# Kernel optimization log

Measured on AMD Instinct MI355X. Metric: run time of the kernel, lower is better.

## Reference

```python
import jax, jax.numpy as jnp
import numpy as np

B, T, DIM, FF, E, TOPK = 2, 2048, 1024, 4096, 8, 2


def setup_inputs() -> dict:
    key = jax.random.key(0)
    k0, k1, k2, k3 = jax.random.split(key, 4)
    x = jax.random.normal(k0, (B, T, DIM), jnp.float32)
    # router weight [E, D] (nn.Linear(dim, num_experts, bias=False))
    Wr = jax.random.normal(k1, (E, DIM), jnp.float32) * (DIM ** -0.5)
    # per-expert FFN weights, stacked: W1 [E, D, FF], W2 [E, FF, D]
    W1 = jax.random.normal(k2, (E, DIM, FF), jnp.float32) * (DIM ** -0.5)
    W2 = jax.random.normal(k3, (E, FF, DIM), jnp.float32) * (FF ** -0.5)
    return {"x": x, "Wr": Wr, "W1": W1, "W2": W2}


def reference(x, Wr, W1, W2):
    """MoEFeedForward.forward, world_size=1, STANDARD implementation.

    Math: per token, top_k experts by router logits, softmax over the top_k
    logits (fp32), y = sum_k w_k * FFN_{e_k}(x). The torch code realizes this
    via sort/permute + per-expert variable-size GEMM + weighted index_add;
    the scatter-add result is identical to the dense masked form below,
    which is the jit-friendly (static-shape) expression.
    """
    Bn, Tn, D = x.shape
    num_experts = Wr.shape[0]
    xf = x.reshape(-1, D)                      # [N, D], N = B*T
    N = xf.shape[0]

    logits = xf @ Wr.T                         # [N, E]
    topw, topi = jax.lax.top_k(logits, TOPK)   # [N, K]
    topw = jax.nn.softmax(topw.astype(jnp.float32), axis=-1).astype(x.dtype)

    # combine weight for each (token, expert): [N, E] (0 if not routed)
    combine = jnp.zeros((N, num_experts), x.dtype)
    combine = combine.at[jnp.arange(N)[:, None], topi].add(topw)

    out = jnp.zeros_like(xf)
    for e in range(num_experts):               # fixed small loop over experts
        h = jax.nn.gelu(xf @ W1[e], approximate=False)  # exact GELU (nn.GELU)
        out = out + combine[:, e:e + 1] * (h @ W2[e])
    return out.reshape(Bn, Tn, D)
```

## Files before the change

kernel.cpp:

```cpp
#include <hip/hip_runtime.h>
#include <hip/hip_bf16.h>
#include <hip/hip_fp16.h>

#define NTOK 4096
#define DIM 1024
#define FF 4096
#define NE 8
#define NSLOT 8192

typedef _Float16 half8 __attribute__((ext_vector_type(8)));
typedef _Float16 half4 __attribute__((ext_vector_type(4)));
typedef float floatx4 __attribute__((ext_vector_type(4)));

__device__ __forceinline__ float gelu_exact(float x) {
    return 0.5f * x * (1.0f + erff(x * 0.70710678118654752f));
}

__device__ __forceinline__ void gl_lds16(const void* g, void* l) {
    __builtin_amdgcn_global_load_lds(
        (const __attribute__((address_space(1))) void*)g,
        (__attribute__((address_space(3))) void*)l, 16, 0, 0);
}

__device__ __forceinline__ void transpose_tile128(const float* __restrict__ s,
                                                  _Float16* __restrict__ d,
                                                  int R, int C, int r0, int c0,
                                                  char* smem) {
    float* t = (float*)smem;
    int tid = threadIdx.x;
    int rr = tid >> 4, cc = (tid & 15) * 4;
#pragma unroll
    for (int i = 0; i < 8; ++i) {
        int r = rr + i * 16;
        float4 v = *(const float4*)(s + (size_t)(r0 + r) * C + c0 + cc);
        *(float4*)(t + r * 64 + (cc ^ (((r >> 3) & 15) << 2))) = v;
    }
    __syncthreads();
#pragma unroll
    for (int j = 0; j < 4; ++j) {
        int chunk = j * 256 + tid;
        int fr = chunk >> 4, ch = chunk & 15;
        half8 v;
#pragma unroll
        for (int u = 0; u < 8; ++u)
            v[u] = (_Float16)t[(ch * 8 + u) * 64 + (fr ^ (ch << 2))];
        *(half8*)(d + (size_t)(c0 + fr) * R + r0 + ch * 8) = v;
    }
}

__global__ __launch_bounds__(256) void k_prep(
    const float* __restrict__ x,
    const float* __restrict__ Wr,
    const float* __restrict__ W1,
    _Float16* __restrict__ w1t,
    _Float16* __restrict__ xh,
    int* __restrict__ counts,
    int* __restrict__ tok_e,
    float* __restrict__ tok_w,
    int* __restrict__ tok_pos) {
    __shared__ char smem[32768];
    int bid = blockIdx.x;
    int tid = threadIdx.x;
    int q = bid / 7, r = bid % 7;
    if (r < 4) {
        int t = q * 4 + r;
        int e = t >> 9, rem = t & 511;
        int r0 = (rem >> 6) << 7, c0 = (rem & 63) << 6;
        transpose_tile128(W1 + (size_t)e * DIM * FF, w1t + (size_t)e * FF * DIM,
                          DIM, FF, r0, c0, smem);
    } else if (r < 6) {
        int i = (q * 2 + (r - 4)) * 2048 + tid * 8;
        float4 a = *(const float4*)(x + i);
        float4 b = *(const float4*)(x + i + 4);
        half8 h;
        h[0] = (_Float16)a.x; h[1] = (_Float16)a.y; h[2] = (_Float16)a.z; h[3] = (_Float16)a.w;
        h[4] = (_Float16)b.x; h[5] = (_Float16)b.y; h[6] = (_Float16)b.z; h[7] = (_Float16)b.w;
        *(half8*)(xh + i) = h;
    } else {
        float* wr = (float*)smem;
        for (int i = tid; i < NE * DIM / 4; i += 256)
            ((float4*)wr)[i] = ((const float4*)Wr)[i];
        __syncthreads();
        int w = tid >> 6, lane = tid & 63;
        int t = q * 4 + w;
        float acc[NE] = {};
        for (int j = 0; j < DIM / 64; ++j) {
            float xv = x[t * DIM + j * 64 + lane];
#pragma unroll
            for (int e = 0; e < NE; ++e)
                acc[e] += xv * wr[e * DIM + j * 64 + lane];
        }
#pragma unroll
        for (int e = 0; e < NE; ++e) {
#pragma unroll
            for (int s = 32; s; s >>= 1) acc[e] += __shfl_xor(acc[e], s, 64);
        }
        if (lane == 0) {
            int b0 = 0; float m0 = acc[0];
#pragma unroll
            for (int e = 1; e < NE; ++e) { if (acc[e] > m0) { m0 = acc[e]; b0 = e; } }
            int b1 = -1; float m1 = -1e30f;
#pragma unroll
            for (int e = 0; e < NE; ++e) { if (e != b0 && acc[e] > m1) { m1 = acc[e]; b1 = e; } }
            float z = __expf(m1 - m0);
            float zz = 1.0f / (1.0f + z);
            int p0 = atomicAdd(&counts[b0], 1);
            int p1 = atomicAdd(&counts[b1], 1);
            tok_e[2 * t] = b0;  tok_e[2 * t + 1] = b1;
            tok_w[2 * t] = zz;  tok_w[2 * t + 1] = z * zz;
            tok_pos[2 * t] = p0; tok_pos[2 * t + 1] = p1;
        }
    }
}

__global__ __launch_bounds__(256) void k_transpose(const float* __restrict__ src,
                                                   _Float16* __restrict__ dst,
                                                   int R, int C) {
    __shared__ float t[64][65];
    int e = blockIdx.z;
    const float* s = src + (size_t)e * R * C;
    _Float16* d = dst + (size_t)e * C * R;
    int r0 = blockIdx.y * 64, c0 = blockIdx.x * 64;
    int tid = threadIdx.x;
    int rr = tid >> 4, cc = (tid & 15) * 4;
#pragma unroll
    for (int i = 0; i < 4; ++i) {
        float4 v = *(const float4*)(s + (size_t)(r0 + rr + i * 16) * C + c0 + cc);
        t[rr + i * 16][cc] = v.x; t[rr + i * 16][cc + 1] = v.y;
        t[rr + i * 16][cc + 2] = v.z; t[rr + i * 16][cc + 3] = v.w;
    }
    __syncthreads();
    int f = tid >> 3, ch = tid & 7;
#pragma unroll
    for (int j = 0; j < 2; ++j) {
        int fr = f + j * 32;
        half8 v;
#pragma unroll
        for (int u = 0; u < 8; ++u) v[u] = (_Float16)t[ch * 8 + u][fr];
        *(half8*)(d + (size_t)(c0 + fr) * R + r0 + ch * 8) = v;
    }
}

__global__ __launch_bounds__(256) void k_prefix_slots(
    const int* __restrict__ counts, int* __restrict__ offs,
    int* __restrict__ tmap256, int* __restrict__ tmap128,
    const int* __restrict__ tok_e, const int* __restrict__ tok_pos,
    int* __restrict__ tok_slot, int* __restrict__ list_tok) {
    __shared__ int soffs[NE];
    if (threadIdx.x == 0) {
        int s = 0, n2 = 0, n1 = 0;
        for (int e = 0; e < NE; ++e) {
            offs[e] = s; soffs[e] = s;
            int c = counts[e];
            for (int mt = 0; mt * 256 < c; ++mt) tmap256[1 + n2++] = (e << 16) | mt;
            for (int mt = 0; mt * 128 < c; ++mt) tmap128[1 + n1++] = (e << 16) | mt;
            s += c;
        }
        offs[NE] = s;
        tmap256[0] = n2;
        tmap128[0] = n1;
    }
    __syncthreads();
    for (int idx = threadIdx.x; idx < NSLOT; idx += 256) {
        int e = tok_e[idx];
        int slot = soffs[e] + tok_pos[idx];
        tok_slot[idx] = slot;
        list_tok[slot] = idx >> 1;
    }
}

template<int K, int NOUT, bool GATHER, bool GELU>
__device__ __forceinline__ void ffn128_body(
    const _Float16* __restrict__ Abase,
    const _Float16* __restrict__ Wbase,
    const int* __restrict__ counts,
    const int* __restrict__ offs,
    const int* __restrict__ list_tok,
    _Float16* __restrict__ Out,
    int e, int mt, int f0, _Float16* lds) {

    int base = offs[e] + mt * 128;
    int valid = counts[e] - mt * 128;

    int tid = threadIdx.x;
    int wid = tid >> 6, lane = tid & 63;

    const char* AB = (const char*)Abase;
    const char* WB = (const char*)(Wbase + (size_t)e * NOUT * K);

    size_t aoff[4]; unsigned boff[4];
#pragma unroll
    for (int i = 0; i < 4; ++i) {
        int g = wid * 256 + i * 64 + lane;
        int r = g >> 3;
        int c = (g & 7) ^ (r & 7);
        int rr = (r < valid) ? r : (valid - 1);
        unsigned arow = GATHER ? (unsigned)list_tok[base + rr] : (unsigned)(base + rr);
        aoff[i] = (size_t)arow * (K * 2) + c * 16;
        boff[i] = (unsigned)(f0 + r) * (unsigned)(K * 2) + c * 16;
    }

    floatx4 acc[4][4];
#pragma unroll
    for (int m = 0; m < 4; ++m)
#pragma unroll
        for (int n = 0; n < 4; ++n) acc[m][n] = (floatx4){0.f, 0.f, 0.f, 0.f};

    int la = lane & 15, lb = lane >> 4;
    int wm = (wid >> 1) * 64, wn = (wid & 1) * 64;

#pragma unroll
    for (int i = 0; i < 4; ++i)
        gl_lds16(AB + aoff[i], lds + wid * 2048 + i * 512);
#pragma unroll
    for (int i = 0; i < 4; ++i)
        gl_lds16(WB + boff[i], lds + 16384 + wid * 2048 + i * 512);
    asm volatile("s_waitcnt vmcnt(0)" ::: "memory");
    __builtin_amdgcn_s_barrier();
    __builtin_amdgcn_sched_barrier(0);

    constexpr int NT = K / 64;
#pragma unroll 2
    for (int t = 0; t < NT; ++t) {
        int cur = t & 1;
        if (t + 1 < NT) {
            size_t kadv = (size_t)(t + 1) * 128;
            _Float16* Ad = lds + (cur ^ 1) * 8192;
            _Float16* Bd = lds + 16384 + (cur ^ 1) * 8192;
#pragma unroll
            for (int i = 0; i < 4; ++i)
                gl_lds16(AB + aoff[i] + kadv, Ad + wid * 2048 + i * 512);
#pragma unroll
            for (int i = 0; i < 4; ++i)
                gl_lds16(WB + boff[i] + kadv, Bd + wid * 2048 + i * 512);
        }
        const _Float16* Ac = lds + cur * 8192;
        const _Float16* Bc = lds + 16384 + cur * 8192;
#pragma unroll
        for (int kk = 0; kk < 2; ++kk) {
            half8 af[4], bf[4];
#pragma unroll
            for (int m = 0; m < 4; ++m) {
                int row = wm + m * 16 + la;
                int c = kk * 4 + lb;
                af[m] = *(const half8*)(Ac + row * 64 + ((c ^ (row & 7)) * 8));
            }
#pragma unroll
            for (int n = 0; n < 4; ++n) {
                int row = wn + n * 16 + la;
                int c = kk * 4 + lb;
                bf[n] = *(const half8*)(Bc + row * 64 + ((c ^ (row & 7)) * 8));
            }
#pragma unroll
            for (int m = 0; m < 4; ++m)
#pragma unroll
                for (int n = 0; n < 4; ++n)
                    acc[m][n] = __builtin_amdgcn_mfma_f32_16x16x32_f16(af[m], bf[n], acc[m][n], 0, 0, 0);
        }
        __builtin_amdgcn_sched_barrier(0);
        asm volatile("s_waitcnt vmcnt(0)" ::: "memory");
        __builtin_amdgcn_s_barrier();
        __builtin_amdgcn_sched_barrier(0);
    }

    _Float16* tw = lds + wid * 4096;
#pragma unroll
    for (int m = 0; m < 4; ++m)
#pragma unroll
        for (int n = 0; n < 4; ++n) {
            floatx4 v = acc[m][n];
#pragma unroll
            for (int i = 0; i < 4; ++i) {
                float fv = v[i];
                if (GELU) fv = gelu_exact(fv);
                tw[(m * 16 + lb * 4 + i) * 64 + n * 16 + la] = (_Float16)fv;
            }
        }
    asm volatile("s_waitcnt lgkmcnt(0)" ::: "memory");
    __builtin_amdgcn_sched_barrier(0);
#pragma unroll
    for (int i = 0; i < 8; ++i) {
        int gi = i * 64 + lane;
        int row = gi >> 3, c8 = gi & 7;
        half8 v = *(const half8*)(tw + gi * 8);
        int trow = wm + row;
        if (trow < valid)
            *(half8*)(Out + (size_t)(base + trow) * NOUT + f0 + wn + c8 * 8) = v;
    }
}

template<int K, int NOUT, bool GATHER, bool GELU>
__global__ __launch_bounds__(256) void k_ffn(
    const _Float16* __restrict__ Abase,
    const _Float16* __restrict__ Wbase,
    const int* __restrict__ tmap,
    const int* __restrict__ counts,
    const int* __restrict__ offs,
    const int* __restrict__ list_tok,
    _Float16* __restrict__ Out) {
    __shared__ _Float16 lds[32768];
    int nt_m = tmap[0];
    if ((int)blockIdx.x >= nt_m) return;
    int ent = tmap[1 + blockIdx.x];
    ffn128_body<K, NOUT, GATHER, GELU>(Abase, Wbase, counts, offs, list_tok, Out,
                                       ent >> 16, ent & 0xffff, blockIdx.y * 128, lds);
}

__global__ __launch_bounds__(256) void k_ffn1_fused(
    const _Float16* __restrict__ xh,
    const _Float16* __restrict__ w1t,
    const int* __restrict__ tmap,
    const int* __restrict__ counts,
    const int* __restrict__ offs,
    const int* __restrict__ list_tok,
    _Float16* __restrict__ hbuf,
    const float* __restrict__ W2,
    _Float16* __restrict__ w2t) {
    __shared__ _Float16 lds[32768];
    int bid = blockIdx.x;
    int q = bid / 10, r = bid % 10;
    if (r < 2) {
        int f = q * 2 + r;
        int nt_m = tmap[0];
        int tile = f >> 5;
        if (tile >= nt_m) return;
        int ent = tmap[1 + tile];
        ffn128_body<DIM, FF, true, true>(xh, w1t, counts, offs, list_tok, hbuf,
                                         ent >> 16, ent & 0xffff, (f & 31) * 128, lds);
    } else {
        int t = q * 8 + (r - 2);
        if (t >= 8 * 32 * 16) return;
        int e = t >> 9, rem = t & 511;
        int r0 = (rem >> 4) << 7, c0 = (rem & 15) << 6;
        transpose_tile128(W2 + (size_t)e * FF * DIM, w2t + (size_t)e * DIM * FF,
                          FF, DIM, r0, c0, (char*)lds);
    }
}

template<int K, int NOUT, int KSPAN, bool GATHER, bool GELU>
__global__ __launch_bounds__(512, 2) void k_ffn256(
    const _Float16* __restrict__ Abase,
    const _Float16* __restrict__ Wbase,
    const int* __restrict__ tmap,
    const int* __restrict__ counts,
    const int* __restrict__ offs,
    const int* __restrict__ list_tok,
    _Float16* __restrict__ Out) {

    int nt_m = tmap[0];
    if ((int)blockIdx.x >= nt_m) return;
    int ent = tmap[1 + blockIdx.x];
    int e = ent >> 16, mt = ent & 0xffff;
    int base = offs[e] + mt * 256;
    int valid = counts[e] - mt * 256;
    int f0 = blockIdx.y * 256;
    int kbase = blockIdx.z * KSPAN;
    Out += (size_t)blockIdx.z * ((size_t)NSLOT * NOUT);

    __shared__ _Float16 lds[65536];

    int tid = threadIdx.x;
    int wid = tid >> 6, lane = tid & 63;

    const char* AB = (const char*)Abase;
    const char* WB = (const char*)(Wbase + (size_t)e * NOUT * K);

    size_t aoff[4]; unsigned boff[4];
#pragma unroll
    for (int i = 0; i < 4; ++i) {
        int g = i * 512 + tid;
        int r = g >> 3;
        int c = (g & 7) ^ (r & 7);
        int rr = (r < valid) ? r : (valid - 1);
        unsigned arow = GATHER ? (unsigned)list_tok[base + rr] : (unsigned)(base + rr);
        aoff[i] = (size_t)arow * (K * 2) + c * 16 + (size_t)kbase * 2;
        boff[i] = (unsigned)(f0 + r) * (unsigned)(K * 2) + c * 16 + (unsigned)kbase * 2;
    }

    floatx4 acc[8][4];
#pragma unroll
    for (int m = 0; m < 8; ++m)
#pragma unroll
        for (int n = 0; n < 4; ++n) acc[m][n] = (floatx4){0.f, 0.f, 0.f, 0.f};

    int la = lane & 15, lb = lane >> 4;
    int wmb = (wid >> 2) * 128, wnb = (wid & 3) * 64;

#pragma unroll
    for (int i = 0; i < 4; ++i)
        gl_lds16(AB + aoff[i], lds + i * 4096 + wid * 512);
#pragma unroll
    for (int i = 0; i < 4; ++i)
        gl_lds16(WB + boff[i], lds + 32768 + i * 4096 + wid * 512);
    asm volatile("s_waitcnt vmcnt(0)" ::: "memory");
    __builtin_amdgcn_s_barrier();
    __builtin_amdgcn_sched_barrier(0);

    constexpr int NT = KSPAN / 64;
#pragma unroll 2
    for (int t = 0; t < NT; ++t) {
        int cur = t & 1;
        if (t + 1 < NT) {
            size_t adv = (size_t)(t + 1) * 128;
            _Float16* Ad = lds + (cur ^ 1) * 16384;
            _Float16* Bd = lds + 32768 + (cur ^ 1) * 16384;
#pragma unroll
            for (int i = 0; i < 4; ++i)
                gl_lds16(AB + aoff[i] + adv, Ad + i * 4096 + wid * 512);
#pragma unroll
            for (int i = 0; i < 4; ++i)
                gl_lds16(WB + boff[i] + adv, Bd + i * 4096 + wid * 512);
        }
        const _Float16* Ac = lds + cur * 16384;
        const _Float16* Bc = lds + 32768 + cur * 16384;
#pragma unroll
        for (int kk = 0; kk < 2; ++kk) {
            half8 af[8], bf[4];
#pragma unroll
            for (int n = 0; n < 4; ++n) {
                int row = wnb + n * 16 + la;
                int c = kk * 4 + lb;
                bf[n] = *(const half8*)(Bc + row * 64 + ((c ^ (row & 7)) * 8));
            }
#pragma unroll
            for (int m = 0; m < 8; ++m) {
                int row = wmb + m * 16 + la;
                int c = kk * 4 + lb;
                af[m] = *(const half8*)(Ac + row * 64 + ((c ^ (row & 7)) * 8));
            }
#pragma unroll
            for (int m = 0; m < 8; ++m)
#pragma unroll
                for (int n = 0; n < 4; ++n)
                    acc[m][n] = __builtin_amdgcn_mfma_f32_16x16x32_f16(af[m], bf[n], acc[m][n], 0, 0, 0);
        }
        __builtin_amdgcn_sched_barrier(0);
        asm volatile("s_waitcnt vmcnt(0)" ::: "memory");
        __builtin_amdgcn_s_barrier();
        __builtin_amdgcn_sched_barrier(0);
    }

    _Float16* tw = lds + wid * 4096;
#pragma unroll
    for (int ps = 0; ps < 2; ++ps) {
#pragma unroll
        for (int fi = 0; fi < 4; ++fi)
#pragma unroll
            for (int nf = 0; nf < 4; ++nf) {
                floatx4 v = acc[ps * 4 + fi][nf];
#pragma unroll
                for (int i2 = 0; i2 < 4; ++i2) {
                    float fv = v[i2];
                    if (GELU) fv = gelu_exact(fv);
                    tw[(fi * 16 + lb * 4 + i2) * 64 + nf * 16 + la] = (_Float16)fv;
                }
            }
        asm volatile("s_waitcnt lgkmcnt(0)" ::: "memory");
        __builtin_amdgcn_sched_barrier(0);
#pragma unroll
        for (int i2 = 0; i2 < 8; ++i2) {
            int gi = i2 * 64 + lane;
            int row = gi >> 3, c8 = gi & 7;
            half8 v = *(const half8*)(tw + gi * 8);
            int trow = wmb + ps * 64 + row;
            if (trow < valid)
                *(half8*)(Out + (size_t)(base + trow) * NOUT + f0 + wnb + c8 * 8) = v;
        }
    }
}

__global__ __launch_bounds__(256) void k_combine(const _Float16* __restrict__ yp,
                                                 const int* __restrict__ tok_slot,
                                                 const float* __restrict__ tok_w,
                                                 float* __restrict__ out,
                                                 int nsplit) {
    int t = blockIdx.x;
    int d = threadIdx.x * 4;
    int s0 = tok_slot[2 * t], s1 = tok_slot[2 * t + 1];
    float w0 = tok_w[2 * t], w1 = tok_w[2 * t + 1];
    float4 sum0 = {0.f, 0.f, 0.f, 0.f}, sum1 = {0.f, 0.f, 0.f, 0.f};
    for (int z = 0; z < nsplit; ++z) {
        const _Float16* p = yp + (size_t)z * NSLOT * DIM;
        half4 y0 = *(const half4*)(p + (size_t)s0 * DIM + d);
        half4 y1 = *(const half4*)(p + (size_t)s1 * DIM + d);
        sum0.x += (float)y0[0]; sum0.y += (float)y0[1];
        sum0.z += (float)y0[2]; sum0.w += (float)y0[3];
        sum1.x += (float)y1[0]; sum1.y += (float)y1[1];
        sum1.z += (float)y1[2]; sum1.w += (float)y1[3];
    }
    float4 o;
    o.x = w0 * sum0.x + w1 * sum1.x;
    o.y = w0 * sum0.y + w1 * sum1.y;
    o.z = w0 * sum0.z + w1 * sum1.z;
    o.w = w0 * sum0.w + w1 * sum1.w;
    *(float4*)(out + (size_t)t * DIM + d) = o;
}

extern "C" void kernel_launch(void* const* d_in, const int* in_sizes, int n_in,
                              void* d_out, int out_size, void* d_ws, size_t ws_size,
                              hipStream_t stream) {
    const float* x  = (const float*)d_in[0];
    const float* Wr = (const float*)d_in[1];
    const float* W1 = (const float*)d_in[2];
    const float* W2 = (const float*)d_in[3];
    float* out = (float*)d_out;

    char* ws = (char*)d_ws;
    _Float16* w1t  = (_Float16*)ws;
    _Float16* xh   = (_Float16*)(ws + 67108864);
    _Float16* hbuf = (_Float16*)(ws + 75497472);
    char* p = ws + 142606336;
    int*   counts   = (int*)p;        p += 1024;
    int*   offs     = (int*)p;        p += 1024;
    int*   tmap256  = (int*)p;        p += 1024;
    int*   tmap128  = (int*)p;        p += 1024;
    int*   tok_e    = (int*)p;        p += NSLOT * 4;
    float* tok_w    = (float*)p;      p += NSLOT * 4;
    int*   tok_pos  = (int*)p;        p += NSLOT * 4;
    int*   tok_slot = (int*)p;        p += NSLOT * 4;
    int*   list_tok = (int*)p;        p += NSLOT * 4;
    const size_t OFF_EXT = 142606336 + 196608;
    const size_t SZ_Y  = (size_t)NSLOT * DIM * 2;
    const size_t SZ_WT = (size_t)NE * DIM * FF * 2;

    bool fused = (ws_size >= OFF_EXT + SZ_WT);

    hipMemsetAsync(counts, 0, 64, stream);
    k_prep<<<7 * 1024, 256, 0, stream>>>(x, Wr, W1, w1t, xh,
                                         counts, tok_e, tok_w, tok_pos);
    k_prefix_slots<<<1, 256, 0, stream>>>(counts, offs, tmap256, tmap128,
                                          tok_e, tok_pos, tok_slot, list_tok);

    if (fused) {
        _Float16* w2t = (_Float16*)(ws + OFF_EXT);
        _Float16* yp  = (_Float16*)ws;
        k_ffn1_fused<<<10 * 1152, 256, 0, stream>>>(
            xh, w1t, tmap128, counts, offs, list_tok, hbuf, W2, w2t);
        k_ffn256<FF, DIM, 1024, false, false>
            <<<dim3(NSLOT / 256 + NE, DIM / 256, 4), 512, 0, stream>>>(
                hbuf, w2t, tmap256, counts, offs, list_tok, yp);
        k_combine<<<NTOK, 256, 0, stream>>>(yp, tok_slot, tok_w, out, 4);
    } else {
        _Float16* w2t = w1t;
        _Float16* yp  = (_Float16*)(ws + OFF_EXT);
        int nsplit = (ws_size >= OFF_EXT + 2 * SZ_Y) ? 2 : 1;
        k_ffn<DIM, FF, true, true>
            <<<dim3(NSLOT / 128 + NE, FF / 128), 256, 0, stream>>>(
                xh, w1t, tmap128, counts, offs, list_tok, hbuf);
        k_transpose<<<dim3(DIM / 64, FF / 64, NE), 256, 0, stream>>>(W2, w2t, FF, DIM);
        if (nsplit == 2) {
            k_ffn256<FF, DIM, 2048, false, false>
                <<<dim3(NSLOT / 256 + NE, DIM / 256, 2), 512, 0, stream>>>(
                    hbuf, w2t, tmap256, counts, offs, list_tok, yp);
        } else {
            k_ffn<FF, DIM, false, false>
                <<<dim3(NSLOT / 128 + NE, DIM / 128), 256, 0, stream>>>(
                    hbuf, w2t, tmap128, counts, offs, list_tok, yp);
        }
        k_combine<<<NTOK, 256, 0, stream>>>(yp, tok_slot, tok_w, out, nsplit);
    }
}
```

Before: 368.9 us.

## Enlarge fused FFN1 GEMM tile to 192 rows and reorder block mapping

Adds a 192-row variant of the expert-grouped FFN1 GEMM body, with a matching 192-row tile map built in the prefix kernel. The fused FFN1/transpose kernel uses it with a smaller grid. Each W1 tile is now reused across more tokens, which cuts weight traffic and LDS-load overhead per MFMA. Block indices are also permuted so that neighbouring workgroups work on different tiles. The cost is more accumulator registers, more LDS per block (80KB), possibly fewer resident blocks, and more padding waste in each expert's last tile.

```diff
diff --git a/kernel.cpp b/kernel.cpp
--- a/kernel.cpp
+++ b/kernel.cpp
@@ -143,21 +143,23 @@
 
 __global__ __launch_bounds__(256) void k_prefix_slots(
     const int* __restrict__ counts, int* __restrict__ offs,
-    int* __restrict__ tmap256, int* __restrict__ tmap128,
+    int* __restrict__ tmap256, int* __restrict__ tmap192, int* __restrict__ tmap128,
     const int* __restrict__ tok_e, const int* __restrict__ tok_pos,
     int* __restrict__ tok_slot, int* __restrict__ list_tok) {
     __shared__ int soffs[NE];
     if (threadIdx.x == 0) {
-        int s = 0, n2 = 0, n1 = 0;
+        int s = 0, n2 = 0, n19 = 0, n1 = 0;
         for (int e = 0; e < NE; ++e) {
             offs[e] = s; soffs[e] = s;
             int c = counts[e];
             for (int mt = 0; mt * 256 < c; ++mt) tmap256[1 + n2++] = (e << 16) | mt;
+            for (int mt = 0; mt * 192 < c; ++mt) tmap192[1 + n19++] = (e << 16) | mt;
             for (int mt = 0; mt * 128 < c; ++mt) tmap128[1 + n1++] = (e << 16) | mt;
             s += c;
         }
         offs[NE] = s;
         tmap256[0] = n2;
+        tmap192[0] = n19;
         tmap128[0] = n1;
     }
     __syncthreads();
@@ -166,6 +168,132 @@
         int slot = soffs[e] + tok_pos[idx];
         tok_slot[idx] = slot;
         list_tok[slot] = idx >> 1;
+    }
+}
+
+template<int K, int NOUT, bool GATHER, bool GELU>
+__device__ __forceinline__ void ffn192_body(
+    const _Float16* __restrict__ Abase,
+    const _Float16* __restrict__ Wbase,
+    const int* __restrict__ counts,
+    const int* __restrict__ offs,
+    const int* __restrict__ list_tok,
+    _Float16* __restrict__ Out,
+    int e, int mt, int f0, _Float16* lds) {
+
+    int base = offs[e] + mt * 192;
+    int valid = counts[e] - mt * 192;
+
+    int tid = threadIdx.x;
+    int wid = tid >> 6, lane = tid & 63;
+
+    const char* AB = (const char*)Abase;
+    const char* WB = (const char*)(Wbase + (size_t)e * NOUT * K);
+
+    size_t aoff[6]; unsigned boff[4];
+#pragma unroll
+    for (int i = 0; i < 6; ++i) {
+        int g = i * 256 + tid;
+        int r = g >> 3;
+        int c = (g & 7) ^ (r & 7);
+        int rr = (r < valid) ? r : (valid - 1);
+        unsigned arow = GATHER ? (unsigned)list_tok[base + rr] : (unsigned)(base + rr);
+        aoff[i] = (size_t)arow * (K * 2) + c * 16;
+    }
+#pragma unroll
+    for (int i = 0; i < 4; ++i) {
+        int g = i * 256 + tid;
+        int r = g >> 3;
+        int c = (g & 7) ^ (r & 7);
+        boff[i] = (unsigned)(f0 + r) * (unsigned)(K * 2) + c * 16;
+    }
+
+    floatx4 acc[6][4];
+#pragma unroll
+    for (int m = 0; m < 6; ++m)
+#pragma unroll
+        for (int n = 0; n < 4; ++n) acc[m][n] = (floatx4){0.f, 0.f, 0.f, 0.f};
+
+    int la = lane & 15, lb = lane >> 4;
+    int wm = (wid >> 1) * 96, wn = (wid & 1) * 64;
+
+#pragma unroll
+    for (int i = 0; i < 6; ++i)
+        gl_lds16(AB + aoff[i], lds + i * 2048 + wid * 512);
+#pragma unroll
+    for (int i = 0; i < 4; ++i)
+        gl_lds16(WB + boff[i], lds + 24576 + i * 2048 + wid * 512);
+    asm volatile("s_waitcnt vmcnt(0)" ::: "memory");
+    __builtin_amdgcn_s_barrier();
+    __builtin_amdgcn_sched_barrier(0);
+
+    constexpr int NT = K / 64;
+#pragma unroll 2
+    for (int t = 0; t < NT; ++t) {
+        int cur = t & 1;
+        if (t + 1 < NT) {
+            size_t kadv = (size_t)(t + 1) * 128;
+            _Float16* Ad = lds + (cur ^ 1) * 12288;
+            _Float16* Bd = lds + 24576 + (cur ^ 1) * 8192;
+#pragma unroll
+            for (int i = 0; i < 6; ++i)
+                gl_lds16(AB + aoff[i] + kadv, Ad + i * 2048 + wid * 512);
+#pragma unroll
+            for (int i = 0; i < 4; ++i)
+                gl_lds16(WB + boff[i] + kadv, Bd + i * 2048 + wid * 512);
+        }
+        const _Float16* Ac = lds + cur * 12288;
+        const _Float16* Bc = lds + 24576 + cur * 8192;
+#pragma unroll
+        for (int kk = 0; kk < 2; ++kk) {
+            half8 af[6], bf[4];
+#pragma unroll
+            for (int m = 0; m < 6; ++m) {
+                int row = wm + m * 16 + la;
+                int c = kk * 4 + lb;
+                af[m] = *(const half8*)(Ac + row * 64 + ((c ^ (row & 7)) * 8));
+            }
+#pragma unroll
+            for (int n = 0; n < 4; ++n) {
+                int row = wn + n * 16 + la;
+                int c = kk * 4 + lb;
+                bf[n] = *(const half8*)(Bc + row * 64 + ((c ^ (row & 7)) * 8));
+            }
+#pragma unroll
+            for (int m = 0; m < 6; ++m)
+#pragma unroll
+                for (int n = 0; n < 4; ++n)
+                    acc[m][n] = __builtin_amdgcn_mfma_f32_16x16x32_f16(af[m], bf[n], acc[m][n], 0, 0, 0);
+        }
+        __builtin_amdgcn_sched_barrier(0);
+        asm volatile("s_waitcnt vmcnt(0)" ::: "memory");
+        __builtin_amdgcn_s_barrier();
+        __builtin_amdgcn_sched_barrier(0);
+    }
+
+    _Float16* tw = lds + wid * 6144;
+#pragma unroll
+    for (int m = 0; m < 6; ++m)
+#pragma unroll
+        for (int n = 0; n < 4; ++n) {
+            floatx4 v = acc[m][n];
+#pragma unroll
+            for (int i = 0; i < 4; ++i) {
+                float fv = v[i];
+                if (GELU) fv = gelu_exact(fv);
+                tw[(m * 16 + lb * 4 + i) * 64 + n * 16 + la] = (_Float16)fv;
+            }
+        }
+    asm volatile("s_waitcnt lgkmcnt(0)" ::: "memory");
+    __builtin_amdgcn_sched_barrier(0);
+#pragma unroll
+    for (int i = 0; i < 12; ++i) {
+        int gi = i * 64 + lane;
+        int row = gi >> 3, c8 = gi & 7;
+        half8 v = *(const half8*)(tw + gi * 8);
+        int trow = wm + row;
+        if (trow < valid)
+            *(half8*)(Out + (size_t)(base + trow) * NOUT + f0 + wn + c8 * 8) = v;
     }
 }
 
@@ -316,16 +444,17 @@
     _Float16* __restrict__ hbuf,
     const float* __restrict__ W2,
     _Float16* __restrict__ w2t) {
-    __shared__ _Float16 lds[32768];
+    __shared__ _Float16 lds[40960];
     int bid = blockIdx.x;
     int q = bid / 10, r = bid % 10;
     if (r < 2) {
-        int f = q * 2 + r;
+        int qp = (q & 3) * 200 + (q >> 2);
+        int f = qp * 2 + r;
         int nt_m = tmap[0];
         int tile = f >> 5;
         if (tile >= nt_m) return;
         int ent = tmap[1 + tile];
-        ffn128_body<DIM, FF, true, true>(xh, w1t, counts, offs, list_tok, hbuf,
+        ffn192_body<DIM, FF, true, true>(xh, w1t, counts, offs, list_tok, hbuf,
                                          ent >> 16, ent & 0xffff, (f & 31) * 128, lds);
     } else {
         int t = q * 8 + (r - 2);
@@ -513,6 +642,7 @@
     int*   counts   = (int*)p;        p += 1024;
     int*   offs     = (int*)p;        p += 1024;
     int*   tmap256  = (int*)p;        p += 1024;
+    int*   tmap192  = (int*)p;        p += 1024;
     int*   tmap128  = (int*)p;        p += 1024;
     int*   tok_e    = (int*)p;        p += NSLOT * 4;
     float* tok_w    = (float*)p;      p += NSLOT * 4;
@@ -528,14 +658,14 @@
     hipMemsetAsync(counts, 0, 64, stream);
     k_prep<<<7 * 1024, 256, 0, stream>>>(x, Wr, W1, w1t, xh,
                                          counts, tok_e, tok_w, tok_pos);
-    k_prefix_slots<<<1, 256, 0, stream>>>(counts, offs, tmap256, tmap128,
+    k_prefix_slots<<<1, 256, 0, stream>>>(counts, offs, tmap256, tmap192, tmap128,
                                           tok_e, tok_pos, tok_slot, list_tok);
 
     if (fused) {
         _Float16* w2t = (_Float16*)(ws + OFF_EXT);
         _Float16* yp  = (_Float16*)ws;
-        k_ffn1_fused<<<10 * 1152, 256, 0, stream>>>(
-            xh, w1t, tmap128, counts, offs, list_tok, hbuf, W2, w2t);
+        k_ffn1_fused<<<10 * 800, 256, 0, stream>>>(
+            xh, w1t, tmap192, counts, offs, list_tok, hbuf, W2, w2t);
         k_ffn256<FF, DIM, 1024, false, false>
             <<<dim3(NSLOT / 256 + NE, DIM / 256, 4), 512, 0, stream>>>(
                 hbuf, w2t, tmap256, counts, offs, list_tok, yp);
```

After: 462.2 us. +25.3%, slower.
